# Kernel optimization log

Hardware: AMD Instinct MI355X
Metric: run time of the kernel (lower is better)

Reference implementation:

```python
import jax, jax.numpy as jnp
import numpy as np

MAX_DELAY = 48          # delay buffer depth
D1 = MAX_DELAY + 1
SIGMA = MAX_DELAY / 2.0
MAX_THINK = 8           # config.max_think_steps
NUM_CLASSES = 63
VOCAB = NUM_CLASSES + 1 # vocab includes think-end token
THINK_END = NUM_CLASSES
H = 512                 # hidden_size
B = 8                   # batch
T = 48                  # encoder time steps


def _calc_credit(tau):
    # relu(-|(d - clip(tau,1,D)) * (1/sigma)^2| + 1/sigma), shape (D1,H,H)
    tc = jnp.clip(tau, 1.0, float(MAX_DELAY))[None]
    d = jnp.arange(D1, dtype=tau.dtype)[:, None, None]
    inv = 1.0 / SIGMA
    return jax.nn.relu(inv - jnp.abs((d - tc) * (inv * inv)))


def _forward(x, wa, ba, lat, tau, we, be, N):
    cm = _calc_credit(tau) * lat[None]   # (D1,H,H), constant across steps
    d_idx = jnp.arange(D1)

    def step_b(buf, ptr, x_t):           # buf (D1,Bx,H), x_t (Bx,VOCAB)
        h_del = jax.lax.dynamic_index_in_dim(buf, ptr, 0, keepdims=False)
        h = jnp.tanh(x_t @ wa.T + ba + h_del)
        scat = jnp.einsum('dhi,bi->dbh', cm, h)
        shifted = scat[(d_idx - ptr) % D1]                      # roll by +ptr along d
        buf = (buf + shifted) * (d_idx != ptr).astype(buf.dtype)[:, None, None]
        y = h_del @ we.T + be
        return buf, (ptr + 1) % D1, y

    def step_1(buf, ptr, x_t):           # per-sample: buf (D1,H), x_t (VOCAB,)
        h_del = jax.lax.dynamic_index_in_dim(buf, ptr, 0, keepdims=False)
        h = jnp.tanh(wa @ x_t + ba + h_del)
        scat = jnp.einsum('dhi,i->dh', cm, h)
        shifted = scat[(d_idx - ptr) % D1]
        buf = (buf + shifted) * (d_idx != ptr).astype(buf.dtype)[:, None]
        y = we @ h_del + be
        return buf, (ptr + 1) % D1, y

    def gumbel_hard(y, k):               # F.gumbel_softmax(tau=1, hard=True)
        u = jax.random.uniform(k, y.shape, minval=1e-9, maxval=1.0)
        logits = y - jnp.log(-jnp.log(u))
        soft = jax.nn.softmax(logits)
        idx = jnp.argmax(logits)
        hard = jax.nn.one_hot(idx, VOCAB, dtype=y.dtype)
        return hard + soft - jax.lax.stop_gradient(soft), idx

    bsz = x.shape[0]
    buf0 = jnp.zeros((D1, bsz, H), x.dtype)

    def enc(carry, x_t):
        buf, ptr = carry
        buf, ptr, _ = step_b(buf, ptr, x_t)
        return (buf, ptr), None

    (buf, ptr), _ = jax.lax.scan(enc, (buf0, jnp.int32(0)), jnp.swapaxes(x, 0, 1))

    def decode_one(buf_i, x_last, key_i):
        # bounded think loop (original while-loop, max MAX_THINK+1 iterations)
        def think(carry, i):
            b, cur, p, done = carry
            nb, np_, y = step_1(b, p, cur)
            ncur, idx = gumbel_hard(y, jax.random.fold_in(key_i, i))
            b = jnp.where(done, b, nb)
            cur = jnp.where(done, cur, ncur)
            p = jnp.where(done, p, np_)
            done = done | (idx == THINK_END) | (i + 1 > MAX_THINK)
            return (b, cur, p, done), None
        (b, cur, p, _), _ = jax.lax.scan(
            think, (buf_i, x_last, ptr, jnp.bool_(False)), jnp.arange(MAX_THINK + 1))

        def dec(carry, j):
            b, cur, p = carry
            b, p, y = step_1(b, p, cur)
            ncur, _ = gumbel_hard(y, jax.random.fold_in(key_i, 10000 + j))
            return (b, ncur, p), y
        _, ys = jax.lax.scan(dec, (b, cur, p), jnp.arange(N))
        return ys                        # (N, VOCAB)

    keys = jax.random.split(jax.random.key(42), bsz)
    ys = jax.vmap(decode_one, in_axes=(1, 0, 0))(buf, x[:, -1, :], keys)
    return ys[:, :, :-1]                 # drop think-end logit


def setup_inputs() -> dict:
    key = jax.random.key(0)
    ks = jax.random.split(key, 6)
    x = jax.random.normal(ks[0], (B, T, VOCAB), dtype=jnp.float32)
    lim_a = (6.0 / (VOCAB + H)) ** 0.5
    w_afferent = jax.random.uniform(ks[1], (H, VOCAB), minval=-lim_a, maxval=lim_a)
    b_afferent = jnp.zeros((H,), jnp.float32)
    lim_l = (6.0 / (H + H)) ** 0.5
    lateral = jax.random.uniform(ks[2], (H, H), minval=-lim_l, maxval=lim_l)
    tau = MAX_DELAY * jax.random.uniform(ks[3], (H, H)) + 1.0
    lim_e = (6.0 / (H + VOCAB)) ** 0.5
    w_efferent = jax.random.uniform(ks[4], (VOCAB, H), minval=-lim_e, maxval=lim_e)
    b_efferent = jnp.zeros((VOCAB,), jnp.float32)
    return {"x": x, "w_afferent": w_afferent, "b_afferent": b_afferent,
            "lateral": lateral, "tau": tau,
            "w_efferent": w_efferent, "b_efferent": b_efferent, "N": T - 3}


def reference(x, w_afferent, b_afferent, lateral, tau, w_efferent, b_efferent, N):
    return _forward(x, w_afferent, b_afferent, lateral, tau, w_efferent, b_efferent, N)
```

## Files before the change

### kernel.cpp

```cpp
#include <hip/hip_runtime.h>
#include <stdint.h>

namespace {

constexpr int H = 512, V = 64, B = 8, T = 48, D1 = 49, NDEC = 45, NSTEP = 102;
constexpr int NBLK = 256, TPB = 512;
constexpr int NG = 8, GMEM = NBLK / NG;

constexpr size_t OFF_PUB = 0;
constexpr size_t OFF_IDX = 2 * 32768;
constexpr size_t OFF_BAR = OFF_IDX + NSTEP * B;
constexpr size_t OFF_YP  = OFF_BAR + 512;
constexpr size_t OFF_XW  = OFF_YP + 8 * 8 * 64;

__device__ __forceinline__ float ldA(const float* p) {
  return __hip_atomic_load(p, __ATOMIC_RELAXED, __HIP_MEMORY_SCOPE_AGENT);
}
__device__ __forceinline__ void stA(float* p, float v) {
  __hip_atomic_store(p, v, __ATOMIC_RELAXED, __HIP_MEMORY_SCOPE_AGENT);
}
__device__ __forceinline__ int ldAi(const int* p) {
  return __hip_atomic_load(p, __ATOMIC_RELAXED, __HIP_MEMORY_SCOPE_AGENT);
}
__device__ __forceinline__ void stAi(int* p, int v) {
  __hip_atomic_store(p, v, __ATOMIC_RELAXED, __HIP_MEMORY_SCOPE_AGENT);
}

__device__ __forceinline__ void tf2x32(uint32_t k0, uint32_t k1,
                                       uint32_t& x0, uint32_t& x1) {
  const uint32_t ks2 = k0 ^ k1 ^ 0x1BD11BDAu;
  x0 += k0; x1 += k1;
#define RR(r) { x0 += x1; x1 = (x1 << (r)) | (x1 >> (32-(r))); x1 ^= x0; }
  RR(13) RR(15) RR(26) RR(6)  x0 += k1;  x1 += ks2 + 1u;
  RR(17) RR(29) RR(16) RR(24) x0 += ks2; x1 += k0 + 2u;
  RR(13) RR(15) RR(26) RR(6)  x0 += k0;  x1 += k1 + 3u;
  RR(17) RR(29) RR(16) RR(24) x0 += k1;  x1 += ks2 + 4u;
  RR(13) RR(15) RR(26) RR(6)  x0 += ks2; x1 += k0 + 5u;
#undef RR
}

__device__ __forceinline__ float gumbel_from_bits(uint32_t bits) {
  float u = __uint_as_float((bits >> 9) | 0x3F800000u) - 1.0f;
  u = u + 1e-9f;
  return -logf(-logf(u));
}

__global__ __launch_bounds__(512) void k_zero(float* __restrict__ ws) {
  int* bar = (int*)ws + OFF_BAR;
  if (threadIdx.x < 512) stAi(&bar[threadIdx.x], 0);
  for (int i = threadIdx.x; i < 32768; i += 512) stA(&ws[i], 0.0f);
}

__device__ __forceinline__ void gbar(int* bar, int grp, int ep) {
  asm volatile("s_waitcnt vmcnt(0)" ::: "memory");
  __syncthreads();
  if (threadIdx.x == 0) {
    int old = __hip_atomic_fetch_add(&bar[16 + 16 * grp], 1,
                                     __ATOMIC_RELAXED, __HIP_MEMORY_SCOPE_AGENT);
    if (((old + 1) & (GMEM - 1)) == 0) {
      int oldG = __hip_atomic_fetch_add(&bar[0], 1,
                                        __ATOMIC_RELAXED, __HIP_MEMORY_SCOPE_AGENT);
      if (((oldG + 1) & (NG - 1)) == 0) {
        #pragma unroll
        for (int q = 0; q < NG; ++q) stAi(&bar[160 + 16 * q], ep);
      }
    }
    int guard = 0;
    while (ldAi(&bar[160 + 16 * grp]) < ep) {
      __builtin_amdgcn_s_sleep(2);
      if (++guard > (1 << 20)) break;
    }
  }
  __syncthreads();
}

__global__ __launch_bounds__(TPB, 4)
void k_main(
    const float* __restrict__ x,  const float* __restrict__ wa,
    const float* __restrict__ ba, const float* __restrict__ lat,
    const float* __restrict__ tau,const float* __restrict__ we,
    const float* __restrict__ be, float* __restrict__ ws,
    float* __restrict__ out) {
  const int blk = blockIdx.x, tid = threadIdx.x;
  const int grp = blk % NG;
  float* pub = ws + OFF_PUB;
  float* yp  = ws + OFF_YP;
  float* xw  = ws + OFF_XW;
  int* idxA = (int*)ws + OFF_IDX;
  int* bar  = (int*)ws + OFF_BAR;

  const int p  = blk >> 5;
  const int g  = blk & 31;
  const int w  = tid >> 6, lane = tid & 63;
  const int cb = p * 64;
  const bool isG0  = (g == 0);
  const bool isFin = (g == 31);
  const int fb = p;

  __shared__ float s_h[8 * 64];
  __shared__ float s_hd2[8 * 64];
  __shared__ float s_tc[16 * 64];
  __shared__ float s_lat[16 * 64];
  __shared__ float s_buf[8 * 16 * 49];
  __shared__ int   s_ptr[8], s_cidx[8], s_done8[8];

  for (int q2 = tid; q2 < 8 * 16 * 49; q2 += TPB) s_buf[q2] = 0.0f;
  for (int q2 = tid; q2 < 16 * 64; q2 += TPB) {
    int hl = q2 >> 6, ii = q2 & 63;
    int ho = g * 16 + hl, i = cb + ii;
    float tv = tau[(size_t)ho * H + i];
    s_tc[q2]  = fminf(fmaxf(tv, 1.0f), 48.0f);
    s_lat[q2] = lat[(size_t)ho * H + i];
  }
  if (tid < 8) { s_ptr[tid] = 0; s_cidx[tid] = 0; s_done8[tid] = 0; }
  if (g < 24) {
    #pragma unroll
    for (int tt = 0; tt < 2; ++tt) {
      int t0 = g * 2 + tt;
      int b = (tid >> 6) & 7, il = tid & 63;
      int j = cb + il;
      const float* xr = x + ((size_t)b * T + t0) * V;
      const float* war = wa + (size_t)j * V;
      float acc = 0.0f;
      #pragma unroll
      for (int v = 0; v < V; v += 4) {
        float4 w4 = *(const float4*)(war + v);
        float4 x4 = *(const float4*)(xr + v);
        acc = fmaf(w4.x, x4.x, acc); acc = fmaf(w4.y, x4.y, acc);
        acc = fmaf(w4.z, x4.z, acc); acc = fmaf(w4.w, x4.w, acc);
      }
      stA(&xw[((size_t)t0 * 8 + b) * 512 + j], acc);
    }
  }
  uint32_t ka = 0u, kb = (uint32_t)fb;
  tf2x32(0u, 42u, ka, kb);

  gbar(bar, grp, 1);

  for (int t = 0; t < NSTEP; ++t) {
    const bool thinkM = (t >= T && t < T + 9);
    const bool decM   = (t >= T + 9);

    if (tid < 8 && t >= 1) {
      const int b = tid;
      const bool prevThink = (t - 1 >= T) && (t - 1 < T + 9);
      const bool aP = prevThink ? (s_done8[b] == 0) : true;
      if (t - 1 >= T) {
        int ix = ldAi(&idxA[(t - 1) * 8 + b]);
        if (aP) s_cidx[b] = ix;
        if (prevThink && (ix == 63 || (t - 1 - T) == 8)) s_done8[b] = 1;
      }
      if (aP) { int pv = s_ptr[b]; s_ptr[b] = (pv + 1 == D1) ? 0 : pv + 1; }
    }
    __syncthreads();

    int actM = 0;
    #pragma unroll
    for (int b = 0; b < B; ++b)
      actM |= ((thinkM ? (s_done8[b] ^ 1) : 1) & 1) << b;

    {
      int il = tid & 63, b = tid >> 6;
      int j = cb + il;
      const float* pr = pub + ((size_t)(t & 1) * 32768 + (size_t)j * 64 + b * 8);
      float p0 = ldA(pr),     p1 = ldA(pr + 1), p2 = ldA(pr + 2), p3 = ldA(pr + 3);
      float p4 = ldA(pr + 4), p5 = ldA(pr + 5), p6 = ldA(pr + 6), p7 = ldA(pr + 7);
      float hd = ((p0 + p1) + (p2 + p3)) + ((p4 + p5) + (p6 + p7));
      if (isG0 && t >= T) s_hd2[b * 64 + il] = hd;
      float acc;
      if (t <= T) {
        int xrow = (t < T) ? t : (T - 1);
        acc = (ba[j] + hd) + ldA(&xw[((size_t)xrow * 8 + b) * 512 + j]);
      } else {
        acc = (ba[j] + hd) + wa[(size_t)j * V + s_cidx[b]];
      }
      s_h[b * 64 + il] = tanhf(acc);
    }
    __syncthreads();

    {
      const float dd = (float)lane;
      const float inv = 1.0f / 24.0f, inv2 = inv * inv;
      float accA[8], accB[8];
      #pragma unroll
      for (int b = 0; b < B; ++b) { accA[b] = 0.0f; accB[b] = 0.0f; }
      const float* tcA = &s_tc[(w * 2) * 64];
      const float* ltA = &s_lat[(w * 2) * 64];
      const float* tcB = &s_tc[(w * 2 + 1) * 64];
      const float* ltB = &s_lat[(w * 2 + 1) * 64];
      #pragma unroll 4
      for (int ii = 0; ii < 64; ii += 4) {
        float4 tA = *(const float4*)(tcA + ii);
        float4 lA = *(const float4*)(ltA + ii);
        float4 tB = *(const float4*)(tcB + ii);
        float4 lB = *(const float4*)(ltB + ii);
        float qA[4], qB[4];
        #pragma unroll
        for (int k = 0; k < 4; ++k) {
          float ta = ((const float*)&tA)[k];
          qA[k] = fmaxf(0.0f, inv - fabsf((dd - ta) * inv2)) * ((const float*)&lA)[k];
          float tb = ((const float*)&tB)[k];
          qB[k] = fmaxf(0.0f, inv - fabsf((dd - tb) * inv2)) * ((const float*)&lB)[k];
        }
        #pragma unroll
        for (int b = 0; b < B; ++b) {
          float4 h4 = *(const float4*)(&s_h[b * 64 + ii]);
          const float* hp = (const float*)&h4;
          #pragma unroll
          for (int k = 0; k < 4; ++k) accA[b] = fmaf(qA[k], hp[k], accA[b]);
          #pragma unroll
          for (int k = 0; k < 4; ++k) accB[b] = fmaf(qB[k], hp[k], accB[b]);
        }
      }
      if (lane >= 1 && lane <= 48) {
        #pragma unroll
        for (int b = 0; b < B; ++b) {
          if ((actM >> b) & 1) {
            int slot = s_ptr[b] + lane; if (slot >= D1) slot -= D1;
            int aA = (b * 16 + w * 2) * 49 + slot;
            float oA = s_buf[aA];
            s_buf[aA] = (lane == 48) ? accA[b] : (oA + accA[b]);
            int aB = (b * 16 + w * 2 + 1) * 49 + slot;
            float oB = s_buf[aB];
            s_buf[aB] = (lane == 48) ? accB[b] : (oB + accB[b]);
          }
        }
      }
    }
    __syncthreads();

    if (tid < 128) {
      int hl = tid >> 3, b = tid & 7;
      int sn = ((actM >> b) & 1) ? s_ptr[b] + 1 : s_ptr[b];
      if (sn >= D1) sn -= D1;
      float val = s_buf[(b * 16 + hl) * 49 + sn];
      stA(&pub[(size_t)((t + 1) & 1) * 32768
               + (size_t)(g * 16 + hl) * 64 + b * 8 + p], val);
    }

    if (isG0 && t >= T) {
      int b = tid >> 6, o = tid & 63;
      const float* wer = we + (size_t)o * H + cb;
      const float* hp  = &s_hd2[b * 64];
      float a2 = 0.0f;
      #pragma unroll
      for (int i2 = 0; i2 < 64; i2 += 4) {
        float4 w4 = *(const float4*)(wer + i2);
        a2 = fmaf(w4.x, hp[i2],     a2); a2 = fmaf(w4.y, hp[i2 + 1], a2);
        a2 = fmaf(w4.z, hp[i2 + 2], a2); a2 = fmaf(w4.w, hp[i2 + 3], a2);
      }
      stA(&yp[(size_t)p * 512 + b * 64 + o], a2);
      asm volatile("s_waitcnt vmcnt(0)" ::: "memory");
      __syncthreads();
      if (tid == 0) stAi(&bar[256 + 16 * p], t + 1);
    }

    if (isFin && t >= T) {
      if (tid < 64) {
        const int o = tid, it = t - T;
        if (o < 8) {
          int guard = 0;
          while (ldAi(&bar[256 + 16 * o]) < t + 1) {
            __builtin_amdgcn_s_sleep(1);
            if (++guard > (1 << 22)) break;
          }
        }
        asm volatile("" ::: "memory");
        const float* ypr = yp + fb * 64 + o;
        float y0 = ldA(ypr),        y1 = ldA(ypr + 512);
        float y2 = ldA(ypr + 1024), y3 = ldA(ypr + 1536);
        float y4 = ldA(ypr + 2048), y5 = ldA(ypr + 2560);
        float y6 = ldA(ypr + 3072), y7 = ldA(ypr + 3584);
        float y = (((y0 + y1) + (y2 + y3)) + ((y4 + y5) + (y6 + y7))) + be[o];
        if (decM && o < V - 1)
          out[((size_t)fb * NDEC + (t - T - 9)) * (V - 1) + o] = y;
        uint32_t data = (it < 9) ? (uint32_t)it : (uint32_t)(10000 + (it - 9));
        uint32_t e = 0u, f = data; tf2x32(ka, kb, e, f);
        uint32_t r0 = 0u, r1 = (uint32_t)o; tf2x32(e, f, r0, r1);
        float bv = y + gumbel_from_bits(r0 ^ r1);
        int bi = o;
        #pragma unroll
        for (int m = 32; m >= 1; m >>= 1) {
          float ov = __shfl_xor(bv, m, 64);
          int   oi = __shfl_xor(bi, m, 64);
          if (ov > bv || (ov == bv && oi < bi)) { bv = ov; bi = oi; }
        }
        if (o == 0) stAi(&idxA[t * 8 + fb], bi);
      }
    }

    gbar(bar, grp, t + 2);
  }
}

}

extern "C" void kernel_launch(void* const* d_in, const int* in_sizes, int n_in,
                              void* d_out, int out_size, void* d_ws, size_t ws_size,
                              hipStream_t stream) {
  (void)in_sizes; (void)n_in; (void)out_size; (void)ws_size;
  const float* x   = (const float*)d_in[0];
  const float* wa  = (const float*)d_in[1];
  const float* ba  = (const float*)d_in[2];
  const float* lat = (const float*)d_in[3];
  const float* tau = (const float*)d_in[4];
  const float* we  = (const float*)d_in[5];
  const float* be  = (const float*)d_in[6];
  float* out = (float*)d_out;
  float* ws  = (float*)d_ws;

  k_zero<<<dim3(1), dim3(512), 0, stream>>>(ws);
  k_main<<<dim3(NBLK), dim3(TPB), 0, stream>>>(x, wa, ba, lat, tau, we, be, ws, out);
}
```

Measured before the change: 1.725 ms.

## Replace per-step grid barrier with point-to-point producer flags and quad-buffered publish

The global barrier at the end of every timestep is removed. Each block now waits only on the 32 per-producer flags of its own partition, plus the sampled-index flags during decoding. The publish buffer and the efferent partial buffer go from double to quad buffering so that blocks can drift apart by more than one step. The efferent partial matvec is moved earlier in the step so the sampling block can proceed sooner. This aims to cut barrier latency and serialization on the per-step critical path, at the cost of more spin-wait polling and tighter correctness reasoning about how far blocks may run ahead.

```diff
diff --git a/kernel.cpp b/kernel.cpp
--- a/kernel.cpp
+++ b/kernel.cpp
@@ -7,11 +7,14 @@
 constexpr int NBLK = 256, TPB = 512;
 constexpr int NG = 8, GMEM = NBLK / NG;
 
-constexpr size_t OFF_PUB = 0;
-constexpr size_t OFF_IDX = 2 * 32768;
-constexpr size_t OFF_BAR = OFF_IDX + NSTEP * B;
-constexpr size_t OFF_YP  = OFF_BAR + 512;
-constexpr size_t OFF_XW  = OFF_YP + 8 * 8 * 64;
+constexpr size_t OFF_PUB  = 0;
+constexpr size_t OFF_IDX  = 131072;
+constexpr size_t OFF_PFLG = 132096;
+constexpr size_t OFF_YPF  = 132352;
+constexpr size_t OFF_YF   = 132416;
+constexpr size_t OFF_BAR  = 132544;
+constexpr size_t OFF_YP   = 133056;
+constexpr size_t OFF_XW   = 149440;
 
 __device__ __forceinline__ float ldA(const float* p) {
   return __hip_atomic_load(p, __ATOMIC_RELAXED, __HIP_MEMORY_SCOPE_AGENT);
@@ -46,8 +49,9 @@
 }
 
 __global__ __launch_bounds__(512) void k_zero(float* __restrict__ ws) {
-  int* bar = (int*)ws + OFF_BAR;
-  if (threadIdx.x < 512) stAi(&bar[threadIdx.x], 0);
+  int* ib = (int*)ws;
+  for (size_t i = OFF_PFLG + threadIdx.x; i < OFF_BAR + 512; i += 512)
+    stAi(&ib[i], 0);
   for (int i = threadIdx.x; i < 32768; i += 512) stA(&ws[i], 0.0f);
 }
 
@@ -82,12 +86,14 @@
     const float* __restrict__ be, float* __restrict__ ws,
     float* __restrict__ out) {
   const int blk = blockIdx.x, tid = threadIdx.x;
-  const int grp = blk % NG;
   float* pub = ws + OFF_PUB;
   float* yp  = ws + OFF_YP;
   float* xw  = ws + OFF_XW;
-  int* idxA = (int*)ws + OFF_IDX;
-  int* bar  = (int*)ws + OFF_BAR;
+  int* idxA  = (int*)ws + OFF_IDX;
+  int* pflag = (int*)ws + OFF_PFLG;
+  int* ypf   = (int*)ws + OFF_YPF;
+  int* yf    = (int*)ws + OFF_YF;
+  int* bar   = (int*)ws + OFF_BAR;
 
   const int p  = blk >> 5;
   const int g  = blk & 31;
@@ -135,11 +141,26 @@
   uint32_t ka = 0u, kb = (uint32_t)fb;
   tf2x32(0u, 42u, ka, kb);
 
-  gbar(bar, grp, 1);
+  gbar(bar, blk % NG, 1);
 
   for (int t = 0; t < NSTEP; ++t) {
     const bool thinkM = (t >= T && t < T + 9);
     const bool decM   = (t >= T + 9);
+    const int needY   = (t - 1 >= T) ? 1 : 0;
+
+    if (tid < 64) {
+      int guard = 0;
+      while (true) {
+        int pred = 1;
+        if (lane < 32)      pred = (ldAi(&pflag[p * 32 + lane]) >= t);
+        else if (lane < 40 && needY) pred = (ldAi(&yf[lane - 32]) >= t - 1);
+        if (__all(pred)) break;
+        __builtin_amdgcn_s_sleep(1);
+        if (++guard > (1 << 22)) break;
+      }
+    }
+    __syncthreads();
+    asm volatile("" ::: "memory");
 
     if (tid < 8 && t >= 1) {
       const int b = tid;
@@ -162,7 +183,7 @@
     {
       int il = tid & 63, b = tid >> 6;
       int j = cb + il;
-      const float* pr = pub + ((size_t)(t & 1) * 32768 + (size_t)j * 64 + b * 8);
+      const float* pr = pub + ((size_t)(t & 3) * 32768 + (size_t)j * 64 + b * 8);
       float p0 = ldA(pr),     p1 = ldA(pr + 1), p2 = ldA(pr + 2), p3 = ldA(pr + 3);
       float p4 = ldA(pr + 4), p5 = ldA(pr + 5), p6 = ldA(pr + 6), p7 = ldA(pr + 7);
       float hd = ((p0 + p1) + (p2 + p3)) + ((p4 + p5) + (p6 + p7));
@@ -177,6 +198,23 @@
       s_h[b * 64 + il] = tanhf(acc);
     }
     __syncthreads();
+
+    if (isG0 && t >= T) {
+      int b = tid >> 6, o = tid & 63;
+      const float* wer = we + (size_t)o * H + cb;
+      const float* hp  = &s_hd2[b * 64];
+      float a2 = 0.0f;
+      #pragma unroll
+      for (int i2 = 0; i2 < 64; i2 += 4) {
+        float4 w4 = *(const float4*)(wer + i2);
+        a2 = fmaf(w4.x, hp[i2],     a2); a2 = fmaf(w4.y, hp[i2 + 1], a2);
+        a2 = fmaf(w4.z, hp[i2 + 2], a2); a2 = fmaf(w4.w, hp[i2 + 3], a2);
+      }
+      stA(&yp[(size_t)(t & 3) * 4096 + (size_t)p * 512 + b * 64 + o], a2);
+      asm volatile("s_waitcnt vmcnt(0)" ::: "memory");
+      __syncthreads();
+      if (tid == 0) stAi(&ypf[p], t);
+    }
 
     {
       const float dd = (float)lane;
@@ -234,62 +272,48 @@
       int sn = ((actM >> b) & 1) ? s_ptr[b] + 1 : s_ptr[b];
       if (sn >= D1) sn -= D1;
       float val = s_buf[(b * 16 + hl) * 49 + sn];
-      stA(&pub[(size_t)((t + 1) & 1) * 32768
+      stA(&pub[(size_t)((t + 1) & 3) * 32768
                + (size_t)(g * 16 + hl) * 64 + b * 8 + p], val);
     }
-
-    if (isG0 && t >= T) {
-      int b = tid >> 6, o = tid & 63;
-      const float* wer = we + (size_t)o * H + cb;
-      const float* hp  = &s_hd2[b * 64];
-      float a2 = 0.0f;
+    asm volatile("s_waitcnt vmcnt(0)" ::: "memory");
+    __syncthreads();
+    if (tid == 0) stAi(&pflag[g * 8 + p], t + 1);
+
+    if (isFin && t >= T && tid < 64) {
+      const int o = tid, it = t - T;
+      if (o < 8) {
+        int guard = 0;
+        while (ldAi(&ypf[o]) < t) {
+          __builtin_amdgcn_s_sleep(1);
+          if (++guard > (1 << 22)) break;
+        }
+      }
+      asm volatile("" ::: "memory");
+      const float* ypr = yp + (size_t)(t & 3) * 4096 + fb * 64 + o;
+      float y0 = ldA(ypr),        y1 = ldA(ypr + 512);
+      float y2 = ldA(ypr + 1024), y3 = ldA(ypr + 1536);
+      float y4 = ldA(ypr + 2048), y5 = ldA(ypr + 2560);
+      float y6 = ldA(ypr + 3072), y7 = ldA(ypr + 3584);
+      float y = (((y0 + y1) + (y2 + y3)) + ((y4 + y5) + (y6 + y7))) + be[o];
+      if (decM && o < V - 1)
+        out[((size_t)fb * NDEC + (t - T - 9)) * (V - 1) + o] = y;
+      uint32_t data = (it < 9) ? (uint32_t)it : (uint32_t)(10000 + (it - 9));
+      uint32_t e = 0u, f = data; tf2x32(ka, kb, e, f);
+      uint32_t r0 = 0u, r1 = (uint32_t)o; tf2x32(e, f, r0, r1);
+      float bv = y + gumbel_from_bits(r0 ^ r1);
+      int bi = o;
       #pragma unroll
-      for (int i2 = 0; i2 < 64; i2 += 4) {
-        float4 w4 = *(const float4*)(wer + i2);
-        a2 = fmaf(w4.x, hp[i2],     a2); a2 = fmaf(w4.y, hp[i2 + 1], a2);
-        a2 = fmaf(w4.z, hp[i2 + 2], a2); a2 = fmaf(w4.w, hp[i2 + 3], a2);
-      }
-      stA(&yp[(size_t)p * 512 + b * 64 + o], a2);
-      asm volatile("s_waitcnt vmcnt(0)" ::: "memory");
-      __syncthreads();
-      if (tid == 0) stAi(&bar[256 + 16 * p], t + 1);
-    }
-
-    if (isFin && t >= T) {
-      if (tid < 64) {
-        const int o = tid, it = t - T;
-        if (o < 8) {
-          int guard = 0;
-          while (ldAi(&bar[256 + 16 * o]) < t + 1) {
-            __builtin_amdgcn_s_sleep(1);
-            if (++guard > (1 << 22)) break;
-          }
-        }
-        asm volatile("" ::: "memory");
-        const float* ypr = yp + fb * 64 + o;
-        float y0 = ldA(ypr),        y1 = ldA(ypr + 512);
-        float y2 = ldA(ypr + 1024), y3 = ldA(ypr + 1536);
-        float y4 = ldA(ypr + 2048), y5 = ldA(ypr + 2560);
-        float y6 = ldA(ypr + 3072), y7 = ldA(ypr + 3584);
-        float y = (((y0 + y1) + (y2 + y3)) + ((y4 + y5) + (y6 + y7))) + be[o];
-        if (decM && o < V - 1)
-          out[((size_t)fb * NDEC + (t - T - 9)) * (V - 1) + o] = y;
-        uint32_t data = (it < 9) ? (uint32_t)it : (uint32_t)(10000 + (it - 9));
-        uint32_t e = 0u, f = data; tf2x32(ka, kb, e, f);
-        uint32_t r0 = 0u, r1 = (uint32_t)o; tf2x32(e, f, r0, r1);
-        float bv = y + gumbel_from_bits(r0 ^ r1);
-        int bi = o;
-        #pragma unroll
-        for (int m = 32; m >= 1; m >>= 1) {
-          float ov = __shfl_xor(bv, m, 64);
-          int   oi = __shfl_xor(bi, m, 64);
-          if (ov > bv || (ov == bv && oi < bi)) { bv = ov; bi = oi; }
-        }
-        if (o == 0) stAi(&idxA[t * 8 + fb], bi);
-      }
-    }
-
-    gbar(bar, grp, t + 2);
+      for (int m = 32; m >= 1; m >>= 1) {
+        float ov = __shfl_xor(bv, m, 64);
+        int   oi = __shfl_xor(bi, m, 64);
+        if (ov > bv || (ov == bv && oi < bi)) { bv = ov; bi = oi; }
+      }
+      if (o == 0) {
+        stAi(&idxA[t * 8 + fb], bi);
+        asm volatile("s_waitcnt vmcnt(0)" ::: "memory");
+        stAi(&yf[fb], t);
+      }
+    }
   }
 }
 
```

After: 1.596 ms. -7.4%, faster.
